# Optimization experiments

Hardware: AMD Instinct MI355X
Metric: run time of the kernel (lower is better)

Reference implementation:

```python
import jax, jax.numpy as jnp
import numpy as np

NB, CIN, COUT, MID, G, K = 16, 128, 256, 128, 8, 64
GP = MID // G  # group_planes = 16
EPS = 1e-5


def _bn(x, g, b, axes):
    # train-mode batchnorm (biased var), channel axis = 1
    m = jnp.mean(x, axes, keepdims=True)
    v = jnp.var(x, axes, keepdims=True)
    sh = (1, -1) + (1,) * (x.ndim - 2)
    return g.reshape(sh) * (x - m) * jax.lax.rsqrt(v + EPS) + b.reshape(sh)


def _axial(x, qkv_w, bq_g, bq_b, bs_g, bs_b, bo_g, bo_b, rel):
    # x: [B, MID, K]; attention along last axis
    B = x.shape[0]
    qkv = _bn(jnp.einsum('oc,bcl->bol', qkv_w, x), bq_g, bq_b, (0, 2))
    qkv = qkv.reshape(B, G, 2 * GP, K)
    q, k, v = qkv[:, :, :GP // 2], qkv[:, :, GP // 2:GP], qkv[:, :, GP:]
    # relative position embedding lookup: rel [2*GP, 2K-1]
    idx = jnp.arange(K)[:, None] - jnp.arange(K)[None, :] + K - 1  # [K,K]
    emb = rel[:, idx]  # [2*GP, K, K]
    q_e, k_e, v_e = emb[:GP // 2], emb[GP // 2:GP], emb[GP:]
    qr = 0.1 * jnp.einsum('bgci,cij->bgij', q, q_e)          # f_qr = 0.1
    kr = 0.1 * jnp.einsum('bgci,cij->bgji', k, k_e)          # f_kr, transpose fused
    qk = jnp.einsum('bgci,bgcj->bgij', q, k)
    sim = jnp.concatenate([qk, qr, kr], axis=1)              # [B, 3G, K, K]
    sim = _bn(sim, bs_g, bs_b, (0, 2, 3)).reshape(B, 3, G, K, K).sum(1)
    sim = jax.nn.softmax(sim, axis=-1)                       # [B, G, K, K]
    sv = jnp.einsum('bgij,bgcj->bgci', sim, v)               # f_sv = 1.0
    sve = 0.1 * jnp.einsum('bgij,cij->bgci', sim, v_e)       # f_sve = 0.1
    out = jnp.concatenate([sv, sve], axis=1).reshape(B, 2 * MID, K)
    out = _bn(out, bo_g, bo_b, (0, 2))
    return out.reshape(B, MID, 2, K).sum(2)                  # [B, MID, K]


def _block(x, c1_w, c1_b, cd_w, cd_b, bn1_g, bn1_b,
           h_qkv_w, h_bq_g, h_bq_b, h_bs_g, h_bs_b, h_bo_g, h_bo_b, h_rel,
           w_qkv_w, w_bq_g, w_bq_b, w_bs_g, w_bs_b, w_bo_g, w_bo_b, w_rel,
           cu_w, cu_b, bn2_g, bn2_b):
    x_out = jnp.einsum('oc,nchw->nohw', c1_w, x) + c1_b[None, :, None, None]
    out = jnp.einsum('oc,nchw->nohw', cd_w, x) + cd_b[None, :, None, None]
    out = jax.nn.relu(_bn(out, bn1_g, bn1_b, (0, 2, 3)))
    N = out.shape[0]
    # height block: x.permute(0,3,1,2) -> [N, W, C, H] -> [N*W, C, H]
    h_in = out.transpose(0, 3, 1, 2).reshape(N * K, MID, K)
    h = _axial(h_in, h_qkv_w, h_bq_g, h_bq_b, h_bs_g, h_bs_b, h_bo_g, h_bo_b, h_rel)
    h = h.reshape(N, K, MID, K).transpose(0, 2, 3, 1)  # [N, C, H, W]
    # width block: x.permute(0,2,1,3) -> [N, H, C, W] -> [N*H, C, W]
    w_in = h.transpose(0, 2, 1, 3).reshape(N * K, MID, K)
    w = _axial(w_in, w_qkv_w, w_bq_g, w_bq_b, w_bs_g, w_bs_b, w_bo_g, w_bo_b, w_rel)
    w = w.reshape(N, K, MID, K).transpose(0, 2, 1, 3)  # [N, C, H, W]
    out = jnp.einsum('oc,nchw->nohw', cu_w, w) + cu_b[None, :, None, None]
    out = _bn(out, bn2_g, bn2_b, (0, 2, 3))
    return out + x_out


def setup_inputs() -> dict:
    key = jax.random.key(0)
    ks = jax.random.split(key, 12)
    d = {}
    d['x'] = jax.random.normal(ks[0], (NB, CIN, K, K), jnp.float32)
    d['c1_w'] = jax.random.normal(ks[1], (COUT, CIN), jnp.float32) * np.sqrt(1.0 / CIN)
    d['c1_b'] = jnp.zeros((COUT,), jnp.float32)
    d['cd_w'] = jax.random.normal(ks[2], (MID, CIN), jnp.float32) * np.sqrt(1.0 / CIN)
    d['cd_b'] = jnp.zeros((MID,), jnp.float32)
    d['bn1_g'] = jnp.ones((MID,), jnp.float32); d['bn1_b'] = jnp.zeros((MID,), jnp.float32)
    for i, p in enumerate(['h_', 'w_']):
        d[p + 'qkv_w'] = jax.random.normal(ks[3 + i], (2 * MID, MID), jnp.float32) * np.sqrt(1.0 / MID)
        d[p + 'bq_g'] = jnp.ones((2 * MID,), jnp.float32); d[p + 'bq_b'] = jnp.zeros((2 * MID,), jnp.float32)
        d[p + 'bs_g'] = jnp.ones((3 * G,), jnp.float32); d[p + 'bs_b'] = jnp.zeros((3 * G,), jnp.float32)
        d[p + 'bo_g'] = jnp.ones((2 * MID,), jnp.float32); d[p + 'bo_b'] = jnp.zeros((2 * MID,), jnp.float32)
        d[p + 'rel'] = jax.random.normal(ks[5 + i], (2 * GP, 2 * K - 1), jnp.float32) * np.sqrt(1.0 / GP)
    d['cu_w'] = jax.random.normal(ks[7], (COUT, MID), jnp.float32) * np.sqrt(1.0 / MID)
    d['cu_b'] = jnp.zeros((COUT,), jnp.float32)
    d['bn2_g'] = jnp.ones((COUT,), jnp.float32); d['bn2_b'] = jnp.zeros((COUT,), jnp.float32)
    return d


def reference(x, c1_w, c1_b, cd_w, cd_b, bn1_g, bn1_b,
              h_qkv_w, h_bq_g, h_bq_b, h_bs_g, h_bs_b, h_bo_g, h_bo_b, h_rel,
              w_qkv_w, w_bq_g, w_bq_b, w_bs_g, w_bs_b, w_bo_g, w_bo_b, w_rel,
              cu_w, cu_b, bn2_g, bn2_b):
    return _block(x, c1_w, c1_b, cd_w, cd_b, bn1_g, bn1_b,
                  h_qkv_w, h_bq_g, h_bq_b, h_bs_g, h_bs_b, h_bo_g, h_bo_b, h_rel,
                  w_qkv_w, w_bq_g, w_bq_b, w_bs_g, w_bs_b, w_bo_g, w_bo_b, w_rel,
                  cu_w, cu_b, bn2_g, bn2_b)
```

## Files before the change

### kernel.cpp

```cpp
#include <hip/hip_runtime.h>


#define NCOPY 64

typedef __attribute__((ext_vector_type(8))) short bf16x8;
typedef __attribute__((ext_vector_type(4))) short bf16x4;
typedef __attribute__((ext_vector_type(4))) float f32x4;
typedef __attribute__((ext_vector_type(2))) float f32x2;

__device__ __forceinline__ float wave_sum(float v){
  #pragma unroll
  for (int o = 32; o; o >>= 1) v += __shfl_xor(v, o, 64);
  return v;
}
__device__ __forceinline__ ushort f2bf(float f){
  union { float f; unsigned u; } v; v.f = f;
  unsigned r = v.u + 0x7FFFu + ((v.u >> 16) & 1u);
  return (ushort)(r >> 16);
}
__device__ __forceinline__ float bf2f(ushort u){
  union { unsigned u; float f; } v; v.u = ((unsigned)u) << 16;
  return v.f;
}

__global__ void k_cvt5(const float* __restrict__ s0, const float* __restrict__ s1,
                       const float* __restrict__ s2, const float* __restrict__ s3,
                       const float* __restrict__ s4, ushort* __restrict__ dst){
  int i = blockIdx.x*256 + threadIdx.x;
  if (i >= 147456) return;
  float v;
  if      (i < 16384)  v = s0[i];
  else if (i < 49152)  v = s1[i-16384];
  else if (i < 81920)  v = s2[i-49152];
  else if (i < 114688) v = s3[i-81920];
  else                 v = s4[i-114688];
  dst[i] = f2bf(v);
}

template<int O, int MODE, int SLOG, int INBF, int OUTBF>
__global__ __launch_bounds__(256) void k_gemm(
    const void* __restrict__ X_, const ushort* __restrict__ Wb,
    const float* __restrict__ bias, void* __restrict__ out_,
    float* __restrict__ acc, const ushort* __restrict__ y2,
    const float* __restrict__ scsh, ushort* __restrict__ vout)
{
  constexpr int RPW = O/4;
  constexpr int NS  = RPW/16;
  __shared__ ushort XT[64*128];

  const int tid = threadIdx.x;
  const int col0 = blockIdx.x << 6;
  const int seg  = col0 >> SLOG;
  const int p0   = col0 & ((1<<SLOG)-1);

  {
    const int col = tid & 63;
    const int kc8 = tid >> 6;
    #pragma unroll
    for (int q = 0; q < 4; ++q){
      int kc = kc8*4 + q;
      int c0 = kc*8;
      bf16x8 pk;
      if constexpr (INBF){
        const ushort* xb = (const ushort*)X_ + (((size_t)seg*128) << SLOG) + p0 + col;
        #pragma unroll
        for (int j = 0; j < 8; ++j)
          pk[j] = (short)xb[(size_t)(c0+j) << SLOG];
      } else {
        const float* xb = (const float*)X_ + (((size_t)seg*128) << SLOG) + p0 + col;
        #pragma unroll
        for (int j = 0; j < 8; ++j)
          pk[j] = (short)f2bf(xb[(size_t)(c0+j) << SLOG]);
      }
      *(bf16x8*)&XT[col*128 + ((kc ^ (col & 15)) << 3)] = pk;
    }
  }
  __syncthreads();

  const int lane = tid & 63;
  const int wid  = tid >> 6;
  const int l15  = lane & 15, lg = lane >> 4;

  f32x4 accr[NS][4];
  #pragma unroll
  for (int s = 0; s < NS; ++s)
    #pragma unroll
    for (int ns = 0; ns < 4; ++ns)
      accr[s][ns] = (f32x4){0.f,0.f,0.f,0.f};

  #pragma unroll
  for (int kk = 0; kk < 4; ++kk){
    bf16x8 af[NS];
    #pragma unroll
    for (int s = 0; s < NS; ++s){
      int m = wid*RPW + s*16 + l15;
      af[s] = *(const bf16x8*)(Wb + (size_t)m*128 + kk*32 + lg*8);
    }
    bf16x8 bfr[4];
    #pragma unroll
    for (int ns = 0; ns < 4; ++ns){
      int ncol  = ns*16 + l15;
      int chunk = kk*4 + lg;
      bfr[ns] = *(const bf16x8*)&XT[ncol*128 + ((chunk ^ l15) << 3)];
    }
    #pragma unroll
    for (int s = 0; s < NS; ++s)
      #pragma unroll
      for (int ns = 0; ns < 4; ++ns)
        accr[s][ns] = __builtin_amdgcn_mfma_f32_16x16x32_bf16(
                        af[s], bfr[ns], accr[s][ns], 0, 0, 0);
  }

  float* accb = (MODE != 2) ? acc + (size_t)(blockIdx.x & (NCOPY-1))*2*O : nullptr;
  #pragma unroll
  for (int s = 0; s < NS; ++s){
    #pragma unroll
    for (int r = 0; r < 4; ++r){
      const int m = wid*RPW + s*16 + lg*4 + r;
      const float bs = (MODE == 0 || MODE == 2) ? bias[m] : 0.f;
      float vsum = 0.f, vsq = 0.f;
      #pragma unroll
      for (int ns = 0; ns < 4; ++ns){
        float v = accr[s][ns][r] + bs;
        if constexpr (MODE == 3){
          const int cm = ((m >> 5) << 4) + (m & 15);
          size_t oidx = (((size_t)seg*128 + cm) << SLOG) + p0 + ns*16 + l15;
          if constexpr (true){
            if ((s & 1) == 0) ((float*)out_)[oidx] = v;
            else              vout[oidx] = f2bf(v);
          }
        } else {
          size_t oidx = (((size_t)seg*O + m) << SLOG) + p0 + ns*16 + l15;
          if (MODE == 2)
            v += fmaf(scsh[m], bf2f(y2[oidx]), scsh[O+m]);
          if constexpr (OUTBF) ((ushort*)out_)[oidx] = f2bf(v);
          else                 ((float*) out_)[oidx] = v;
        }
        vsum += v; vsq = fmaf(v, v, vsq);
      }
      if (MODE != 2){
        #pragma unroll
        for (int o2 = 1; o2 < 16; o2 <<= 1){
          vsum += __shfl_xor(vsum, o2, 64);
          vsq  += __shfl_xor(vsq , o2, 64);
        }
        if (l15 == 0){
          atomicAdd(&accb[m],   vsum);
          atomicAdd(&accb[O+m], vsq);
        }
      }
    }
  }
}

__global__ void k_finalize(const float* __restrict__ acc, const float* __restrict__ g,
    const float* __restrict__ b, float* __restrict__ scsh, int C, float invcnt)
{
  int c = blockIdx.x*blockDim.x + threadIdx.x;
  if (c >= C) return;
  float s = 0.f, s2 = 0.f;
  #pragma unroll 4
  for (int k2 = 0; k2 < NCOPY; ++k2){
    s  += acc[(size_t)k2*2*C + c];
    s2 += acc[(size_t)k2*2*C + C + c];
  }
  float mean = s*invcnt;
  float var  = s2*invcnt - mean*mean;
  float sc = g[c]*rsqrtf(var + 1e-5f);
  scsh[c]   = sc;
  scsh[C+c] = fmaf(-mean, sc, b[c]);
}

__global__ __launch_bounds__(256) void k_trans_bnrelu(const ushort* __restrict__ out0,
    const float* __restrict__ scsh, ushort* __restrict__ hin)
{
  __shared__ float t[64][65];
  const int c = blockIdx.x, n = blockIdx.y;
  const int tx = threadIdx.x, ty = threadIdx.y;
  const float sc = scsh[c], sh = scsh[128+c];
  const ushort* src = out0 + ((size_t)n*128 + c)*4096;
  #pragma unroll
  for (int r = 0; r < 16; ++r){
    int h = ty + r*4;
    t[h][tx] = bf2f(src[h*64 + tx]);
  }
  __syncthreads();
  ushort* dst = hin + (size_t)(n*64)*8192 + (size_t)c*64;
  #pragma unroll
  for (int r = 0; r < 16; ++r){
    int w_ = ty + r*4;
    float vv = fmaf(sc, t[tx][w_], sh);
    dst[(size_t)w_*8192 + tx] = f2bf(fmaxf(vv, 0.f));
  }
}

__global__ __launch_bounds__(256) void k_prep_rel2(const float* __restrict__ relh,
    const float* __restrict__ relw, float* __restrict__ rwh, float* __restrict__ rww)
{
  const float* rel = (blockIdx.x & 2) ? relw : relh;
  float* rw        = (blockIdx.x & 2) ? rww  : rwh;
  const int side = blockIdx.x & 1;
  const float* base = rel + side*8*127;
  float* Wout = rw + side*4096;
  float* Sout = rw + 8192 + side*512;
  const int tid = threadIdx.y*64 + threadIdx.x;
  for (int idx = tid; idx < 4096; idx += 256){
    int pr = idx >> 6, i = idx & 63;
    int c = pr >> 3, c2 = pr & 7;
    const float* r1 = base + c*127 + i;
    const float* r2 = base + c2*127 + i;
    float s = 0.f;
    #pragma unroll 8
    for (int u = 0; u < 64; ++u) s = fmaf(r1[u], r2[u], s);
    Wout[idx] = s;
  }
  for (int idx = tid; idx < 512; idx += 256){
    int c = idx >> 6, i = idx & 63;
    const float* r1 = base + c*127 + i;
    float s = 0.f;
    #pragma unroll 8
    for (int u = 0; u < 64; ++u) s += r1[u];
    Sout[idx] = s;
  }
}

__global__ __launch_bounds__(256, 4) void k_att_stats(const float* __restrict__ qk32,
    const float* __restrict__ bq, const float* __restrict__ rw, float* __restrict__ accsim)
{
  __shared__ float WqS[4096], WkS[4096], SqS[512], SkS[512];
  const int b = blockIdx.x;
  const int tx = threadIdx.x, ty = threadIdx.y;
  const int tid = ty*64 + tx;
  for (int idx = tid; idx < 4096; idx += 256){ WqS[idx] = rw[idx]; WkS[idx] = rw[4096+idx]; }
  for (int idx = tid; idx < 512;  idx += 256){ SqS[idx] = rw[8192+idx]; SkS[idx] = rw[8704+idx]; }
  __syncthreads();
  float* accb = accsim + (size_t)(b & (NCOPY-1)) * 48;
  const int i = tx;
  const int l15 = tx & 15, lg = tx >> 4;
  const short one_bf = (short)0x3F80;
  const bf16x8 ones = {one_bf,one_bf,one_bf,one_bf,one_bf,one_bf,one_bf,one_bf};

  #pragma unroll
  for (int gi = 0; gi < 2; ++gi){
    const int g = ty*2 + gi;
    float q[8], k[8];
    #pragma unroll
    for (int c = 0; c < 8; ++c){
      int oq = g*32 + c, ok = oq + 8;
      q[c] = fmaf(bq[oq], qk32[((size_t)b*128 + g*16 + c    )*64 + i], bq[256+oq]);
      k[c] = fmaf(bq[ok], qk32[((size_t)b*128 + g*16 + 8 + c)*64 + i], bq[256+ok]);
    }
    const int och = g*32 + l15;
    const float gsc = bq[och], gsh = bq[256+och];
    const float* src = &qk32[((size_t)b*128 + g*16 + l15)*64 + lg*8];
    bf16x8 a0, a1;
    #pragma unroll
    for (int j = 0; j < 8; ++j) a0[j] = (short)f2bf(fmaf(gsc, src[j],      gsh));
    #pragma unroll
    for (int j = 0; j < 8; ++j) a1[j] = (short)f2bf(fmaf(gsc, src[32 + j], gsh));
    f32x4 G = (f32x4){0.f,0.f,0.f,0.f};
    f32x4 R = (f32x4){0.f,0.f,0.f,0.f};
    G = __builtin_amdgcn_mfma_f32_16x16x32_bf16(a0, a0, G, 0, 0, 0);
    G = __builtin_amdgcn_mfma_f32_16x16x32_bf16(a1, a1, G, 0, 0, 0);
    R = __builtin_amdgcn_mfma_f32_16x16x32_bf16(a0, ones, R, 0, 0, 0);
    R = __builtin_amdgcn_mfma_f32_16x16x32_bf16(a1, ones, R, 0, 0, 0);
    float ss = 0.f, sqk = 0.f;
    const bool gq_lane = (l15 < 8) && (lg < 2);
    const bool r_lane  = (l15 == 0) && (lg < 2);
    #pragma unroll
    for (int r = 0; r < 4; ++r){
      float gsw = __shfl_xor(G[r], 40, 64);
      float rsw = __shfl_xor(R[r], 32, 64);
      if (gq_lane) ss  = fmaf(G[r], gsw, ss);
      if (r_lane)  sqk = fmaf(R[r], rsw, sqk);
    }
    float aq = 0.f, ak = 0.f, aq2 = 0.f, ak2 = 0.f;
    #pragma unroll
    for (int c = 0; c < 8; ++c){
      aq = fmaf(q[c], SqS[c*64 + i], aq);
      ak = fmaf(k[c], SkS[c*64 + i], ak);
    }
    #pragma unroll
    for (int c = 0; c < 8; ++c){
      #pragma unroll
      for (int c2 = c; c2 < 8; ++c2){
        float w2 = (c2 == c) ? 1.f : 2.f;
        aq2 = fmaf(w2*q[c]*q[c2], WqS[(c*8+c2)*64 + i], aq2);
        ak2 = fmaf(w2*k[c]*k[c2], WkS[(c*8+c2)*64 + i], ak2);
      }
    }
    sqk = wave_sum(sqk);  ss  = wave_sum(ss);
    aq  = wave_sum(aq);   ak  = wave_sum(ak);
    aq2 = wave_sum(aq2);  ak2 = wave_sum(ak2);
    if (tx == 0){
      atomicAdd(&accb[g],      sqk);       atomicAdd(&accb[24+g],    ss);
      atomicAdd(&accb[8+g],    0.1f*aq);   atomicAdd(&accb[24+8+g],  0.01f*aq2);
      atomicAdd(&accb[16+g],   0.1f*ak);   atomicAdd(&accb[24+16+g], 0.01f*ak2);
    }
  }
}

__global__ __launch_bounds__(256) void k_att2(const float* __restrict__ qk32,
    const ushort* __restrict__ vbf, const float* __restrict__ bq,
    const float* __restrict__ rel, const float* __restrict__ simsc,
    ushort* __restrict__ svout, float* __restrict__ accbo)
{
  __shared__ __align__(16) char smem[38144];
  float* P32  = (float*)(smem);
  float* REQT = (float*)(smem + 16896);
  float* REKT = (float*)(smem + 23040);
  float* KT   = (float*)(smem + 29184);
  float* RINV = (float*)(smem + 37888);

  const int b = blockIdx.x, g = blockIdx.y;
  const int tx = threadIdx.x, ty = threadIdx.y;
  const int tid = ty*64 + tx;
  const float scq  = simsc[g];
  const float scr_ = 0.1f*simsc[8+g];
  const float sck_ = 0.1f*simsc[16+g];

  if (tid < 128){
    int j = tid & 63, h = tid >> 6;
    f32x4 kv;
    #pragma unroll
    for (int e = 0; e < 4; ++e){
      int o = g*32 + 8 + h*4 + e;
      kv[e] = fmaf(bq[o], qk32[((size_t)b*128 + g*16 + 8 + h*4 + e)*64 + j], bq[256+o]);
    }
    *(f32x4*)(KT + j*8 + h*4) = kv;
  }
  if (tid < 254){
    int side = tid >= 127;
    int d = tid - side*127;
    float rs = side ? sck_ : scr_;
    float* dst = (side ? REKT : REQT) + d*12;
    f32x4 r0, r1;
    #pragma unroll
    for (int e = 0; e < 4; ++e) r0[e] = rel[(side*8 + e)*127 + d]*rs;
    #pragma unroll
    for (int e = 0; e < 4; ++e) r1[e] = rel[(side*8 + 4 + e)*127 + d]*rs;
    *(f32x4*)dst = r0; *(f32x4*)(dst+4) = r1;
  }
  {
    int c = tid >> 4, j4 = (tid & 15)*4;
    int o = g*32 + 16 + c;
    float gsc = bq[o], gsh = bq[256+o];
    const ushort* src = &vbf[((size_t)b*128 + g*16 + c)*64 + j4];
    bf16x4 pv;
    #pragma unroll
    for (int e = 0; e < 4; ++e) pv[e] = (short)f2bf(fmaf(gsc, bf2f(src[e]), gsh));
    *(bf16x4*)(smem + 31232 + c*144 + (((j4>>3) ^ (c&7))<<4) + (j4&7)*2) = pv;
  }
  {
    int c = tid >> 4, d8 = (tid & 15)*8;
    const float* rsrc = &rel[(16+c)*127 + d8];
    bf16x8 pk;
    #pragma unroll
    for (int e = 0; e < 8; ++e){
      int d = d8 + e;
      pk[e] = (d < 127) ? (short)f2bf(0.1f*rsrc[e]) : (short)0;
    }
    *(bf16x8*)(smem + 33536 + c*272 + (((d8>>3) ^ (c&15))<<4)) = pk;
  }
  float q8[8], qs8[8];
  #pragma unroll
  for (int c = 0; c < 8; ++c){
    int o = g*32 + c;
    float qv = fmaf(bq[o], qk32[((size_t)b*128 + g*16 + c)*64 + tx], bq[256+o]);
    q8[c] = qv; qs8[c] = scq*qv;
  }
  __syncthreads();

  {
    const int j0 = ty*16;
    const f32x2* q2  = (const f32x2*)q8;
    const f32x2* qs2 = (const f32x2*)qs8;
    #pragma unroll
    for (int t = 0; t < 16; ++t){
      const int j = j0 + t;
      const f32x2* kt = (const f32x2*)(KT + j*8);
      const f32x2* rq = (const f32x2*)(REQT + (tx - j + 63)*12);
      const f32x2* rk = (const f32x2*)(REKT + (j - tx + 63)*12);
      f32x2 a2 = (f32x2){0.f, 0.f};
      #pragma unroll
      for (int c2 = 0; c2 < 4; ++c2){
        f32x2 ktv = kt[c2];
        a2 = __builtin_elementwise_fma(qs2[c2], ktv,    a2);
        a2 = __builtin_elementwise_fma(q2[c2],  rq[c2], a2);
        a2 = __builtin_elementwise_fma(ktv,     rk[c2], a2);
      }
      P32[tx*66 + j] = a2.x + a2.y;
    }
  }
  __syncthreads();

  float e0[16];
  const int row = tid >> 2, sl = tid & 3;
  {
    const float* prow = &P32[row*66 + sl*16];
    #pragma unroll
    for (int e = 0; e < 16; ++e) e0[e] = prow[e];
    float m0 = fmaxf(fmaxf(e0[0],e0[1]),  fmaxf(e0[2],e0[3]));
    float m1 = fmaxf(fmaxf(e0[4],e0[5]),  fmaxf(e0[6],e0[7]));
    float m2 = fmaxf(fmaxf(e0[8],e0[9]),  fmaxf(e0[10],e0[11]));
    float m3 = fmaxf(fmaxf(e0[12],e0[13]),fmaxf(e0[14],e0[15]));
    float m = fmaxf(fmaxf(m0,m1), fmaxf(m2,m3));
    m = fmaxf(m, __shfl_xor(m, 1, 64));
    m = fmaxf(m, __shfl_xor(m, 2, 64));
    float s = 0.f;
    #pragma unroll
    for (int e = 0; e < 16; ++e){ float ex = __expf(e0[e]-m); e0[e]=ex; s += ex; }
    s += __shfl_xor(s, 1, 64);
    s += __shfl_xor(s, 2, 64);
    __syncthreads();
    {
      f32x4 z = (f32x4){0.f,0.f,0.f,0.f};
      float* zp = (float*)(smem + 8192 + tid*64);
      *(f32x4*)(zp+0) = z; *(f32x4*)(zp+4) = z;
      *(f32x4*)(zp+8) = z; *(f32x4*)(zp+12) = z;
    }
    if (sl == 0) RINV[row] = 1.0f/s;
    __syncthreads();
    bf16x8 pk0, pk1;
    #pragma unroll
    for (int e = 0; e < 8; ++e){ pk0[e] = (short)f2bf(e0[e]); pk1[e] = (short)f2bf(e0[8+e]); }
    char* pbbase = smem + 0 + row*128;
    *(bf16x8*)(pbbase + (((2*sl    ) ^ (row&7))<<4)) = pk0;
    *(bf16x8*)(pbbase + (((2*sl + 1) ^ (row&7))<<4)) = pk1;
    char* ppbase = smem + 8192 + row*256;
    #pragma unroll
    for (int e = 0; e < 16; ++e){
      int j = sl*16 + e, d = row - j + 63;
      *(ushort*)(ppbase + (((d>>3) ^ (row&15))<<4) + (d&7)*2) = f2bf(e0[e]);
    }
  }
  __syncthreads();

  {
    const int l15 = tx & 15, lg = tx >> 4;
    const int i0 = ty*16;
    const int rowA = i0 + l15;
    char* pbA = smem + 0    + rowA*128;
    char* ppA = smem + 8192 + rowA*256;
    char* vbB = smem + 31232 + l15*144;
    char* reB = smem + 33536 + l15*272;
    f32x4 accv = (f32x4){0.f,0.f,0.f,0.f};
    f32x4 acce = (f32x4){0.f,0.f,0.f,0.f};
    #pragma unroll
    for (int kk = 0; kk < 2; ++kk){
      bf16x8 a  = *(bf16x8*)(pbA + (((kk*4+lg) ^ (rowA&7))<<4));
      bf16x8 bb = *(bf16x8*)(vbB + (((kk*4+lg) ^ (l15&7))<<4));
      accv = __builtin_amdgcn_mfma_f32_16x16x32_bf16(a, bb, accv, 0, 0, 0);
    }
    #pragma unroll
    for (int kk = 0; kk < 4; ++kk){
      bf16x8 a  = *(bf16x8*)(ppA + (((kk*4+lg) ^ (rowA&15))<<4));
      bf16x8 bb = *(bf16x8*)(reB + (((kk*4+lg) ^ (l15&15))<<4));
      acce = __builtin_amdgcn_mfma_f32_16x16x32_bf16(a, bb, acce, 0, 0, 0);
    }
    f32x4 ri4 = *(f32x4*)(smem + 37888 + (i0 + lg*4)*4);
    float* accb = accbo + (size_t)(b & (NCOPY-1)) * 512;
    {
      bf16x4 vb4;
      float vsum = 0.f, vsq = 0.f;
      #pragma unroll
      for (int r = 0; r < 4; ++r){
        float v = accv[r]*ri4[r];
        vb4[r] = (short)f2bf(v); vsum += v; vsq = fmaf(v, v, vsq);
      }
      int ch = g*16 + l15;
      *(bf16x4*)&svout[((size_t)b*256 + ch)*64 + i0 + lg*4] = vb4;
      vsum += __shfl_xor(vsum, 16, 64); vsum += __shfl_xor(vsum, 32, 64);
      vsq  += __shfl_xor(vsq , 16, 64); vsq  += __shfl_xor(vsq , 32, 64);
      if (lg == 0){ atomicAdd(&accb[ch], vsum); atomicAdd(&accb[256+ch], vsq); }
    }
    {
      bf16x4 vb4;
      float vsum = 0.f, vsq = 0.f;
      #pragma unroll
      for (int r = 0; r < 4; ++r){
        float v = acce[r]*ri4[r];
        vb4[r] = (short)f2bf(v); vsum += v; vsq = fmaf(v, v, vsq);
      }
      int ch = 128 + g*16 + l15;
      *(bf16x4*)&svout[((size_t)b*256 + ch)*64 + i0 + lg*4] = vb4;
      vsum += __shfl_xor(vsum, 16, 64); vsum += __shfl_xor(vsum, 32, 64);
      vsq  += __shfl_xor(vsq , 16, 64); vsq  += __shfl_xor(vsq , 32, 64);
      if (lg == 0){ atomicAdd(&accb[ch], vsum); atomicAdd(&accb[256+ch], vsq); }
    }
  }
}

__global__ __launch_bounds__(256) void k_pairT(const ushort* __restrict__ sv,
    const float* __restrict__ bo, ushort* __restrict__ win)
{
  __shared__ float t[64][65];
  const int c = blockIdx.x, n = blockIdx.y;
  const int tx = threadIdx.x, ty = threadIdx.y;
  const float s0 = bo[2*c], s1 = bo[2*c+1];
  const float sh = bo[256 + 2*c] + bo[256 + 2*c + 1];
  const ushort* base = sv + (size_t)(n*64)*256*64;
  #pragma unroll
  for (int r = 0; r < 16; ++r){
    int w_ = ty + r*4;
    float v0 = bf2f(base[((size_t)w_*256 + 2*c    )*64 + tx]);
    float v1 = bf2f(base[((size_t)w_*256 + 2*c + 1)*64 + tx]);
    t[w_][tx] = fmaf(s0, v0, fmaf(s1, v1, sh));
  }
  __syncthreads();
  ushort* dst = win + (size_t)(n*64)*8192 + (size_t)c*64;
  #pragma unroll
  for (int r = 0; r < 16; ++r){
    int h_ = ty + r*4;
    dst[(size_t)h_*8192 + tx] = f2bf(t[tx][h_]);
  }
}

__global__ __launch_bounds__(256) void k_pair_w(const ushort* __restrict__ sv,
    const float* __restrict__ bo, ushort* __restrict__ wbuf)
{
  const int m = blockIdx.x, n = blockIdx.y;
  const int tx = threadIdx.x, ty = threadIdx.y;
  const float s0 = bo[2*m], s1 = bo[2*m+1];
  const float sh = bo[256 + 2*m] + bo[256 + 2*m + 1];
  #pragma unroll
  for (int r = 0; r < 16; ++r){
    int h = ty + r*4;
    float v0 = bf2f(sv[((size_t)(n*64+h)*256 + 2*m    )*64 + tx]);
    float v1 = bf2f(sv[((size_t)(n*64+h)*256 + 2*m + 1)*64 + tx]);
    wbuf[((size_t)(n*128+m)*64 + h)*64 + tx] = f2bf(fmaf(s0, v0, fmaf(s1, v1, sh)));
  }
}


extern "C" void kernel_launch(void* const* d_in, const int* in_sizes, int n_in,
                              void* d_out, int out_size, void* d_ws, size_t ws_size,
                              hipStream_t stream)
{
  const float* x     = (const float*)d_in[0];
  const float* c1_w  = (const float*)d_in[1];
  const float* c1_b  = (const float*)d_in[2];
  const float* cd_w  = (const float*)d_in[3];
  const float* cd_b  = (const float*)d_in[4];
  const float* bn1_g = (const float*)d_in[5];
  const float* bn1_b = (const float*)d_in[6];
  const float* h_qkv = (const float*)d_in[7];
  const float* h_bqg = (const float*)d_in[8];
  const float* h_bqb = (const float*)d_in[9];
  const float* h_bsg = (const float*)d_in[10];
  const float* h_bsb = (const float*)d_in[11];
  const float* h_bog = (const float*)d_in[12];
  const float* h_bob = (const float*)d_in[13];
  const float* h_rel = (const float*)d_in[14];
  const float* w_qkv = (const float*)d_in[15];
  const float* w_bqg = (const float*)d_in[16];
  const float* w_bqb = (const float*)d_in[17];
  const float* w_bsg = (const float*)d_in[18];
  const float* w_bsb = (const float*)d_in[19];
  const float* w_bog = (const float*)d_in[20];
  const float* w_bob = (const float*)d_in[21];
  const float* w_rel = (const float*)d_in[22];
  const float* cu_w  = (const float*)d_in[23];
  const float* cu_b  = (const float*)d_in[24];
  const float* bn2_g = (const float*)d_in[25];
  const float* bn2_b = (const float*)d_in[26];
  float* out = (float*)d_out;
  char* ws = (char*)d_ws;

  ushort* OUT0  = (ushort*)(ws + 0);
  ushort* HIN   = (ushort*)(ws + (32ull<<20));
  float*  QK32H = (float*)(ws + (64ull<<20));
  ushort* VBFH  = (ushort*)(ws + (96ull<<20));
  ushort* SVO   = (ushort*)(ws + 0);
  ushort* WIN   = (ushort*)(ws + (64ull<<20));
  float*  QK32W = (float*)(ws + (96ull<<20));
  ushort* VBFW  = (ushort*)(ws + (128ull<<20));
  ushort* WBUF  = (ushort*)(ws + (64ull<<20));
  ushort* Y2    = (ushort*)(ws + (96ull<<20));
  float*  ST    = (float*)(ws + (160ull<<20));

  float* ACC_BN1 = ST;
  float* ACC_BQ  = ST + 16384;
  float* ACC_SIM = ST + 49152;
  float* ACC_BO  = ST + 52224;
  float* ACC_BQW = ST + 84992;
  float* ACC_SIMW= ST + 117760;
  float* ACC_BOW = ST + 120832;
  float* ACC_BN2 = ST + 153600;
  float* SCB     = ST + 186368;
  float* SC_BN1 = SCB;        float* SC_BQ  = SCB + 256;
  float* SC_SIM = SCB + 768;  float* SC_BO  = SCB + 816;
  float* SC_BQW = SCB + 1328; float* SC_SIMW= SCB + 1840;
  float* SC_BOW = SCB + 1888; float* SC_BN2 = SCB + 2400;
  float* RWH  = ST + 189280;
  float* RWW  = ST + 198496;
  ushort* CDBF = (ushort*)(ST + 207712);
  ushort* QHBF = CDBF + 16384;
  ushort* QWBF = CDBF + 49152;
  ushort* CUBF = CDBF + 81920;
  ushort* C1BF = CDBF + 114688;

  hipMemsetAsync(ST, 0, 186368*sizeof(float), stream);

  const dim3 blk(64,4);
  const float inv64k = 1.f/65536.f;
  const float invsim = 1.f/4194304.f;

  k_cvt5<<<576, 256, 0, stream>>>(cd_w, h_qkv, w_qkv, cu_w, c1_w, CDBF);
  k_prep_rel2<<<4, blk, 0, stream>>>(h_rel, w_rel, RWH, RWW);

  k_gemm<128,0,12,0,1><<<1024, 256, 0, stream>>>(x, CDBF, cd_b, OUT0, ACC_BN1, nullptr, nullptr, nullptr);
  k_finalize<<<1, 128, 0, stream>>>(ACC_BN1, bn1_g, bn1_b, SC_BN1, 128, inv64k);
  k_trans_bnrelu<<<dim3(128,16), blk, 0, stream>>>(OUT0, SC_BN1, HIN);

  k_gemm<256,3,6,1,0><<<1024, 256, 0, stream>>>(HIN, QHBF, nullptr, QK32H, ACC_BQ, nullptr, nullptr, VBFH);
  k_finalize<<<1, 256, 0, stream>>>(ACC_BQ, h_bqg, h_bqb, SC_BQ, 256, inv64k);
  k_att_stats<<<1024, blk, 0, stream>>>(QK32H, SC_BQ, RWH, ACC_SIM);
  k_finalize<<<1, 32, 0, stream>>>(ACC_SIM, h_bsg, h_bsb, SC_SIM, 24, invsim);
  k_att2<<<dim3(1024,8), blk, 0, stream>>>(QK32H, VBFH, SC_BQ, h_rel, SC_SIM, SVO, ACC_BO);
  k_finalize<<<1, 256, 0, stream>>>(ACC_BO, h_bog, h_bob, SC_BO, 256, inv64k);
  k_pairT<<<dim3(128,16), blk, 0, stream>>>(SVO, SC_BO, WIN);

  k_gemm<256,3,6,1,0><<<1024, 256, 0, stream>>>(WIN, QWBF, nullptr, QK32W, ACC_BQW, nullptr, nullptr, VBFW);
  k_finalize<<<1, 256, 0, stream>>>(ACC_BQW, w_bqg, w_bqb, SC_BQW, 256, inv64k);
  k_att_stats<<<1024, blk, 0, stream>>>(QK32W, SC_BQW, RWW, ACC_SIMW);
  k_finalize<<<1, 32, 0, stream>>>(ACC_SIMW, w_bsg, w_bsb, SC_SIMW, 24, invsim);
  k_att2<<<dim3(1024,8), blk, 0, stream>>>(QK32W, VBFW, SC_BQW, w_rel, SC_SIMW, SVO, ACC_BOW);
  k_finalize<<<1, 256, 0, stream>>>(ACC_BOW, w_bog, w_bob, SC_BOW, 256, inv64k);
  k_pair_w<<<dim3(128,16), blk, 0, stream>>>(SVO, SC_BOW, WBUF);

  k_gemm<256,0,12,1,1><<<1024, 256, 0, stream>>>(WBUF, CUBF, cu_b, Y2, ACC_BN2, nullptr, nullptr, nullptr);
  k_finalize<<<1, 256, 0, stream>>>(ACC_BN2, bn2_g, bn2_b, SC_BN2, 256, inv64k);
  k_gemm<256,2,12,0,0><<<1024, 256, 0, stream>>>(x, C1BF, c1_b, out, nullptr, Y2, SC_BN2, nullptr);
}
```

Measured before the change: 394.8 us.

## Vectorize transpose kernels and keep softmax scores in registers in att2

The transpose and pairing kernels (k_trans_bnrelu, k_pairT, k_pair_w) now load and store two bf16 values per 32-bit access, launched as flat 256-thread blocks, which halves the number of global memory transactions. In k_att2 the score matrix is no longer staged through a float LDS buffer. Each thread keeps its 16 scores in registers, and the row max and sum are reduced through small shared arrays across the four waves. This frees LDS and drops one round-trip per score, at the cost of extra barriers and a repacked LDS layout.

```diff
diff --git a/kernel.cpp b/kernel.cpp
--- a/kernel.cpp
+++ b/kernel.cpp
@@ -125,10 +125,8 @@
         if constexpr (MODE == 3){
           const int cm = ((m >> 5) << 4) + (m & 15);
           size_t oidx = (((size_t)seg*128 + cm) << SLOG) + p0 + ns*16 + l15;
-          if constexpr (true){
-            if ((s & 1) == 0) ((float*)out_)[oidx] = v;
-            else              vout[oidx] = f2bf(v);
-          }
+          if ((s & 1) == 0) ((float*)out_)[oidx] = v;
+          else              vout[oidx] = f2bf(v);
         } else {
           size_t oidx = (((size_t)seg*O + m) << SLOG) + p0 + ns*16 + l15;
           if (MODE == 2)
@@ -174,23 +172,27 @@
 __global__ __launch_bounds__(256) void k_trans_bnrelu(const ushort* __restrict__ out0,
     const float* __restrict__ scsh, ushort* __restrict__ hin)
 {
-  __shared__ float t[64][65];
+  __shared__ float t[64][66];
   const int c = blockIdx.x, n = blockIdx.y;
-  const int tx = threadIdx.x, ty = threadIdx.y;
+  const int tid = threadIdx.x;
   const float sc = scsh[c], sh = scsh[128+c];
-  const ushort* src = out0 + ((size_t)n*128 + c)*4096;
-  #pragma unroll
-  for (int r = 0; r < 16; ++r){
-    int h = ty + r*4;
-    t[h][tx] = bf2f(src[h*64 + tx]);
-  }
-  __syncthreads();
-  ushort* dst = hin + (size_t)(n*64)*8192 + (size_t)c*64;
-  #pragma unroll
-  for (int r = 0; r < 16; ++r){
-    int w_ = ty + r*4;
-    float vv = fmaf(sc, t[tx][w_], sh);
-    dst[(size_t)w_*8192 + tx] = f2bf(fmaxf(vv, 0.f));
+  const uint* src = (const uint*)(out0 + ((size_t)n*128 + c)*4096);
+  #pragma unroll
+  for (int r = 0; r < 8; ++r){
+    int u = tid + r*256;
+    uint a = src[u];
+    f32x2 vv; vv.x = bf2f((ushort)a); vv.y = bf2f((ushort)(a >> 16));
+    *(f32x2*)&t[u >> 5][(u & 31)*2] = vv;
+  }
+  __syncthreads();
+  uint* dst = (uint*)(hin + (size_t)(n*64)*8192 + (size_t)c*64);
+  #pragma unroll
+  for (int r = 0; r < 8; ++r){
+    int u = tid + r*256;
+    int w = u >> 5, hp = u & 31;
+    float v0 = fmaxf(fmaf(sc, t[2*hp    ][w], sh), 0.f);
+    float v1 = fmaxf(fmaf(sc, t[2*hp + 1][w], sh), 0.f);
+    dst[(size_t)w*4096 + hp] = ((uint)f2bf(v1) << 16) | f2bf(v0);
   }
 }
 
@@ -305,12 +307,13 @@
     const float* __restrict__ rel, const float* __restrict__ simsc,
     ushort* __restrict__ svout, float* __restrict__ accbo)
 {
-  __shared__ __align__(16) char smem[38144];
-  float* P32  = (float*)(smem);
-  float* REQT = (float*)(smem + 16896);
-  float* REKT = (float*)(smem + 23040);
-  float* KT   = (float*)(smem + 29184);
-  float* RINV = (float*)(smem + 37888);
+  __shared__ __align__(16) char smem[32768];
+  float* REQT = (float*)(smem);
+  float* REKT = (float*)(smem + 6144);
+  float* KT   = (float*)(smem + 12288);
+  float* MP   = (float*)(smem + 30720);
+  float* SP   = (float*)(smem + 31744);
+  float* RINV = (float*)(smem + 30720);
 
   const int b = blockIdx.x, g = blockIdx.y;
   const int tx = threadIdx.x, ty = threadIdx.y;
@@ -349,7 +352,7 @@
     bf16x4 pv;
     #pragma unroll
     for (int e = 0; e < 4; ++e) pv[e] = (short)f2bf(fmaf(gsc, bf2f(src[e]), gsh));
-    *(bf16x4*)(smem + 31232 + c*144 + (((j4>>3) ^ (c&7))<<4) + (j4&7)*2) = pv;
+    *(bf16x4*)(smem + 24576 + c*128 + (((j4>>3) ^ (c&7))<<4) + (j4&7)*2) = pv;
   }
   {
     int c = tid >> 4, d8 = (tid & 15)*8;
@@ -360,7 +363,7 @@
       int d = d8 + e;
       pk[e] = (d < 127) ? (short)f2bf(0.1f*rsrc[e]) : (short)0;
     }
-    *(bf16x8*)(smem + 33536 + c*272 + (((d8>>3) ^ (c&15))<<4)) = pk;
+    *(bf16x8*)(smem + 26624 + c*256 + (((d8>>3) ^ (c&15))<<4)) = pk;
   }
   float q8[8], qs8[8];
   #pragma unroll
@@ -371,6 +374,7 @@
   }
   __syncthreads();
 
+  float acc[16];
   {
     const int j0 = ty*16;
     const f32x2* q2  = (const f32x2*)q8;
@@ -389,49 +393,47 @@
         a2 = __builtin_elementwise_fma(q2[c2],  rq[c2], a2);
         a2 = __builtin_elementwise_fma(ktv,     rk[c2], a2);
       }
-      P32[tx*66 + j] = a2.x + a2.y;
-    }
-  }
-  __syncthreads();
-
-  float e0[16];
-  const int row = tid >> 2, sl = tid & 3;
-  {
-    const float* prow = &P32[row*66 + sl*16];
-    #pragma unroll
-    for (int e = 0; e < 16; ++e) e0[e] = prow[e];
-    float m0 = fmaxf(fmaxf(e0[0],e0[1]),  fmaxf(e0[2],e0[3]));
-    float m1 = fmaxf(fmaxf(e0[4],e0[5]),  fmaxf(e0[6],e0[7]));
-    float m2 = fmaxf(fmaxf(e0[8],e0[9]),  fmaxf(e0[10],e0[11]));
-    float m3 = fmaxf(fmaxf(e0[12],e0[13]),fmaxf(e0[14],e0[15]));
-    float m = fmaxf(fmaxf(m0,m1), fmaxf(m2,m3));
-    m = fmaxf(m, __shfl_xor(m, 1, 64));
-    m = fmaxf(m, __shfl_xor(m, 2, 64));
+      acc[t] = a2.x + a2.y;
+    }
+  }
+  {
+    float m0 = fmaxf(fmaxf(acc[0],acc[1]),  fmaxf(acc[2],acc[3]));
+    float m1 = fmaxf(fmaxf(acc[4],acc[5]),  fmaxf(acc[6],acc[7]));
+    float m2 = fmaxf(fmaxf(acc[8],acc[9]),  fmaxf(acc[10],acc[11]));
+    float m3 = fmaxf(fmaxf(acc[12],acc[13]),fmaxf(acc[14],acc[15]));
+    MP[ty*64 + tx] = fmaxf(fmaxf(m0,m1), fmaxf(m2,m3));
+  }
+  __syncthreads();
+
+  {
+    f32x4 z = (f32x4){0.f,0.f,0.f,0.f};
+    float* zp = (float*)(smem + 8192 + tid*64);
+    *(f32x4*)(zp+0) = z; *(f32x4*)(zp+4) = z;
+    *(f32x4*)(zp+8) = z; *(f32x4*)(zp+12) = z;
+  }
+  {
+    float mrow = fmaxf(fmaxf(MP[tx], MP[64+tx]), fmaxf(MP[128+tx], MP[192+tx]));
     float s = 0.f;
     #pragma unroll
-    for (int e = 0; e < 16; ++e){ float ex = __expf(e0[e]-m); e0[e]=ex; s += ex; }
-    s += __shfl_xor(s, 1, 64);
-    s += __shfl_xor(s, 2, 64);
-    __syncthreads();
-    {
-      f32x4 z = (f32x4){0.f,0.f,0.f,0.f};
-      float* zp = (float*)(smem + 8192 + tid*64);
-      *(f32x4*)(zp+0) = z; *(f32x4*)(zp+4) = z;
-      *(f32x4*)(zp+8) = z; *(f32x4*)(zp+12) = z;
-    }
-    if (sl == 0) RINV[row] = 1.0f/s;
-    __syncthreads();
+    for (int t = 0; t < 16; ++t){ float ex = __expf(acc[t]-mrow); acc[t] = ex; s += ex; }
+    SP[ty*64 + tx] = s;
+  }
+  __syncthreads();
+
+  if (ty == 0)
+    RINV[tx] = 1.0f / ((SP[tx] + SP[64+tx]) + (SP[128+tx] + SP[192+tx]));
+  {
     bf16x8 pk0, pk1;
     #pragma unroll
-    for (int e = 0; e < 8; ++e){ pk0[e] = (short)f2bf(e0[e]); pk1[e] = (short)f2bf(e0[8+e]); }
-    char* pbbase = smem + 0 + row*128;
-    *(bf16x8*)(pbbase + (((2*sl    ) ^ (row&7))<<4)) = pk0;
-    *(bf16x8*)(pbbase + (((2*sl + 1) ^ (row&7))<<4)) = pk1;
-    char* ppbase = smem + 8192 + row*256;
+    for (int e = 0; e < 8; ++e){ pk0[e] = (short)f2bf(acc[e]); pk1[e] = (short)f2bf(acc[8+e]); }
+    char* pbbase = smem + 0 + tx*128;
+    *(bf16x8*)(pbbase + (((2*ty    ) ^ (tx&7))<<4)) = pk0;
+    *(bf16x8*)(pbbase + (((2*ty + 1) ^ (tx&7))<<4)) = pk1;
+    char* ppbase = smem + 8192 + tx*256;
     #pragma unroll
     for (int e = 0; e < 16; ++e){
-      int j = sl*16 + e, d = row - j + 63;
-      *(ushort*)(ppbase + (((d>>3) ^ (row&15))<<4) + (d&7)*2) = f2bf(e0[e]);
+      int j = ty*16 + e, d = tx - j + 63;
+      *(ushort*)(ppbase + (((d>>3) ^ (tx&15))<<4) + (d&7)*2) = f2bf(acc[e]);
     }
   }
   __syncthreads();
@@ -442,8 +444,8 @@
     const int rowA = i0 + l15;
     char* pbA = smem + 0    + rowA*128;
     char* ppA = smem + 8192 + rowA*256;
-    char* vbB = smem + 31232 + l15*144;
-    char* reB = smem + 33536 + l15*272;
+    char* vbB = smem + 24576 + l15*128;
+    char* reB = smem + 26624 + l15*256;
     f32x4 accv = (f32x4){0.f,0.f,0.f,0.f};
     f32x4 acce = (f32x4){0.f,0.f,0.f,0.f};
     #pragma unroll
@@ -458,7 +460,7 @@
       bf16x8 bb = *(bf16x8*)(reB + (((kk*4+lg) ^ (l15&15))<<4));
       acce = __builtin_amdgcn_mfma_f32_16x16x32_bf16(a, bb, acce, 0, 0, 0);
     }
-    f32x4 ri4 = *(f32x4*)(smem + 37888 + (i0 + lg*4)*4);
+    f32x4 ri4 = *(f32x4*)(smem + 30720 + (i0 + lg*4)*4);
     float* accb = accbo + (size_t)(b & (NCOPY-1)) * 512;
     {
       bf16x4 vb4;
@@ -494,25 +496,34 @@
 __global__ __launch_bounds__(256) void k_pairT(const ushort* __restrict__ sv,
     const float* __restrict__ bo, ushort* __restrict__ win)
 {
-  __shared__ float t[64][65];
+  __shared__ float t[64][66];
   const int c = blockIdx.x, n = blockIdx.y;
-  const int tx = threadIdx.x, ty = threadIdx.y;
+  const int tid = threadIdx.x;
   const float s0 = bo[2*c], s1 = bo[2*c+1];
   const float sh = bo[256 + 2*c] + bo[256 + 2*c + 1];
   const ushort* base = sv + (size_t)(n*64)*256*64;
   #pragma unroll
-  for (int r = 0; r < 16; ++r){
-    int w_ = ty + r*4;
-    float v0 = bf2f(base[((size_t)w_*256 + 2*c    )*64 + tx]);
-    float v1 = bf2f(base[((size_t)w_*256 + 2*c + 1)*64 + tx]);
-    t[w_][tx] = fmaf(s0, v0, fmaf(s1, v1, sh));
-  }
-  __syncthreads();
-  ushort* dst = win + (size_t)(n*64)*8192 + (size_t)c*64;
-  #pragma unroll
-  for (int r = 0; r < 16; ++r){
-    int h_ = ty + r*4;
-    dst[(size_t)h_*8192 + tx] = f2bf(t[tx][h_]);
+  for (int r = 0; r < 8; ++r){
+    int u = tid + r*256;
+    int w = u >> 5, hp = u & 31;
+    uint a = *(const uint*)&base[((size_t)w*256 + 2*c    )*64 + 2*hp];
+    uint bwd = *(const uint*)&base[((size_t)w*256 + 2*c + 1)*64 + 2*hp];
+    float a0 = bf2f((ushort)a),   a1 = bf2f((ushort)(a >> 16));
+    float b0 = bf2f((ushort)bwd), b1 = bf2f((ushort)(bwd >> 16));
+    f32x2 vv;
+    vv.x = fmaf(s0, a0, fmaf(s1, b0, sh));
+    vv.y = fmaf(s0, a1, fmaf(s1, b1, sh));
+    *(f32x2*)&t[w][2*hp] = vv;
+  }
+  __syncthreads();
+  uint* dst = (uint*)(win + (size_t)(n*64)*8192 + (size_t)c*64);
+  #pragma unroll
+  for (int r = 0; r < 8; ++r){
+    int u = tid + r*256;
+    int h = u >> 5, wp = u & 31;
+    float v0 = t[2*wp    ][h];
+    float v1 = t[2*wp + 1][h];
+    dst[(size_t)h*4096 + wp] = ((uint)f2bf(v1) << 16) | f2bf(v0);
   }
 }
 
@@ -520,15 +531,23 @@
     const float* __restrict__ bo, ushort* __restrict__ wbuf)
 {
   const int m = blockIdx.x, n = blockIdx.y;
-  const int tx = threadIdx.x, ty = threadIdx.y;
+  const int tid = threadIdx.x;
   const float s0 = bo[2*m], s1 = bo[2*m+1];
   const float sh = bo[256 + 2*m] + bo[256 + 2*m + 1];
-  #pragma unroll
-  for (int r = 0; r < 16; ++r){
-    int h = ty + r*4;
-    float v0 = bf2f(sv[((size_t)(n*64+h)*256 + 2*m    )*64 + tx]);
-    float v1 = bf2f(sv[((size_t)(n*64+h)*256 + 2*m + 1)*64 + tx]);
-    wbuf[((size_t)(n*128+m)*64 + h)*64 + tx] = f2bf(fmaf(s0, v0, fmaf(s1, v1, sh)));
+  const uint* p0 = (const uint*)(sv + ((size_t)(n*64)*256 + 2*m    )*64);
+  const uint* p1 = (const uint*)(sv + ((size_t)(n*64)*256 + 2*m + 1)*64);
+  uint* dst = (uint*)(wbuf + ((size_t)(n*128 + m)*64)*64);
+  #pragma unroll
+  for (int r = 0; r < 8; ++r){
+    int u = tid + r*256;
+    int h = u >> 5, wp = u & 31;
+    uint a = p0[(size_t)h*8192 + wp];
+    uint bwd = p1[(size_t)h*8192 + wp];
+    float a0 = bf2f((ushort)a),   a1 = bf2f((ushort)(a >> 16));
+    float b0 = bf2f((ushort)bwd), b1 = bf2f((ushort)(bwd >> 16));
+    float r0 = fmaf(s0, a0, fmaf(s1, b0, sh));
+    float r1 = fmaf(s0, a1, fmaf(s1, b1, sh));
+    dst[(size_t)u] = ((uint)f2bf(r1) << 16) | f2bf(r0);
   }
 }
 
@@ -611,7 +630,7 @@
 
   k_gemm<128,0,12,0,1><<<1024, 256, 0, stream>>>(x, CDBF, cd_b, OUT0, ACC_BN1, nullptr, nullptr, nullptr);
   k_finalize<<<1, 128, 0, stream>>>(ACC_BN1, bn1_g, bn1_b, SC_BN1, 128, inv64k);
-  k_trans_bnrelu<<<dim3(128,16), blk, 0, stream>>>(OUT0, SC_BN1, HIN);
+  k_trans_bnrelu<<<dim3(128,16), 256, 0, stream>>>(OUT0, SC_BN1, HIN);
 
   k_gemm<256,3,6,1,0><<<1024, 256, 0, stream>>>(HIN, QHBF, nullptr, QK32H, ACC_BQ, nullptr, nullptr, VBFH);
   k_finalize<<<1, 256, 0, stream>>>(ACC_BQ, h_bqg, h_bqb, SC_BQ, 256, inv64k);
@@ -619,7 +638,7 @@
   k_finalize<<<1, 32, 0, stream>>>(ACC_SIM, h_bsg, h_bsb, SC_SIM, 24, invsim);
   k_att2<<<dim3(1024,8), blk, 0, stream>>>(QK32H, VBFH, SC_BQ, h_rel, SC_SIM, SVO, ACC_BO);
   k_finalize<<<1, 256, 0, stream>>>(ACC_BO, h_bog, h_bob, SC_BO, 256, inv64k);
-  k_pairT<<<dim3(128,16), blk, 0, stream>>>(SVO, SC_BO, WIN);
+  k_pairT<<<dim3(128,16), 256, 0, stream>>>(SVO, SC_BO, WIN);
 
   k_gemm<256,3,6,1,0><<<1024, 256, 0, stream>>>(WIN, QWBF, nullptr, QK32W, ACC_BQW, nullptr, nullptr, VBFW);
   k_finalize<<<1, 256, 0, stream>>>(ACC_BQW, w_bqg, w_bqb, SC_BQW, 256, inv64k);
@@ -627,7 +646,7 @@
   k_finalize<<<1, 32, 0, stream>>>(ACC_SIMW, w_bsg, w_bsb, SC_SIMW, 24, invsim);
   k_att2<<<dim3(1024,8), blk, 0, stream>>>(QK32W, VBFW, SC_BQW, w_rel, SC_SIMW, SVO, ACC_BOW);
   k_finalize<<<1, 256, 0, stream>>>(ACC_BOW, w_bog, w_bob, SC_BOW, 256, inv64k);
-  k_pair_w<<<dim3(128,16), blk, 0, stream>>>(SVO, SC_BOW, WBUF);
+  k_pair_w<<<dim3(128,16), 256, 0, stream>>>(SVO, SC_BOW, WBUF);
 
   k_gemm<256,0,12,1,1><<<1024, 256, 0, stream>>>(WBUF, CUBF, cu_b, Y2, ACC_BN2, nullptr, nullptr, nullptr);
   k_finalize<<<1, 256, 0, stream>>>(ACC_BN2, bn2_g, bn2_b, SC_BN2, 256, inv64k);
```

New measurement: 375.6 us. -4.9%, faster.
